# Kernel tuning notes

Hardware: AMD Instinct MI355X
Metric: run time of the kernel (lower is better)

The kernel has to match this reference:

```python
import jax, jax.numpy as jnp
import numpy as np

MAX_PEAKS = 8192        # static bound for data-dependent nonzero
HEATMAP_ALPHA = 0.9998  # alphas[0]
LOGITS_ALPHA = 0.3      # alphas[2]
WIN = 32                # window size (pad 16 on each side)
NMS_MIN2, NMS_MAX2 = 1.0, 25.0  # squared-dist band: 1 < d < 5
TOPK = (1, 1, 6, 6, 2)  # per-class selection counts from forward()
H = W = 4096


def setup_inputs() -> dict:
    key = jax.random.key(0)
    k1, k2, k3, k4, k5, k6 = jax.random.split(key, 6)
    heatmap = jax.random.uniform(k1, (H, W), dtype=jnp.float32)
    image = jax.random.normal(k2, (1, 3, H, W), dtype=jnp.float32)
    label_W = jax.random.normal(k3, (3 * WIN * WIN, 5), dtype=jnp.float32) * 0.02
    label_b = jax.random.normal(k4, (5,), dtype=jnp.float32) * 0.02
    dir_W = jax.random.normal(k5, (3 * WIN * WIN, 2), dtype=jnp.float32) * 0.02
    dir_b = jax.random.normal(k6, (2,), dtype=jnp.float32) * 0.02
    return {"heatmap": heatmap, "image": image, "label_W": label_W,
            "label_b": label_b, "dir_W": dir_W, "dir_b": dir_b}


def _clamp_alpha(x, alpha):
    x = jnp.clip(x, 0.0, 1.0)
    return jnp.where(x < alpha, 0.0, x)


def _peak_detection(hm):
    # 4-neighbor strict local maxima (same as torch shifted-slice trick)
    b = jnp.pad(hm, 1)
    c = b[1:-1, 1:-1]
    left, right = b[1:-1, 2:], b[1:-1, :-2]
    up, down = b[2:, 1:-1], b[:-2, 1:-1]
    peaks = (c > left) & (c > right) & (c > up) & (c > down)
    ys, xs = jnp.nonzero(peaks, size=MAX_PEAKS, fill_value=-1)
    valid = ys >= 0
    coords = jnp.stack([ys, xs], axis=1)  # [K,2] int, row-major like torch.nonzero
    # Original loop iterates over the ORIGINAL coords tensor (Python iterator is
    # bound before reassignment), so the suppression is order-independent:
    # drop c iff exists original peak p with 1 < dist(c,p) < 5.
    cf = coords.astype(jnp.float32)
    n2 = jnp.sum(cf * cf, axis=1)
    d2 = n2[:, None] + n2[None, :] - 2.0 * (cf @ cf.T)  # [K,K] squared dists
    reject = jnp.any((d2 > NMS_MIN2) & (d2 < NMS_MAX2) & valid[None, :], axis=1)
    return coords, valid & ~reject


def _build_windows(img, coords):
    pad = jnp.pad(img, ((0, 0), (0, 0), (16, 16), (16, 16)))
    starts = jnp.clip(coords, 0)  # padded slots (-1) read window 0; masked later
    def grab(p):
        return jax.lax.dynamic_slice(pad, (0, 0, p[0], p[1]), (1, 3, WIN, WIN))[0]
    return jax.vmap(grab)(starts)  # [K,3,32,32]


def reference(heatmap, image, label_W, label_b, dir_W, dir_b):
    hm = _clamp_alpha(heatmap, HEATMAP_ALPHA)
    coords, keep = _peak_detection(hm)
    windows = _build_windows(image, coords)            # [K,3,32,32]
    feats = windows.reshape(MAX_PEAKS, -1)             # [K,3072]
    logp = jax.nn.log_softmax(feats @ label_W + label_b, axis=-1)
    probs = jnp.exp(logp)                              # torch.exp(self.label(windows))
    scores = jnp.max(probs, axis=-1)
    labels = jnp.argmax(probs, axis=-1)
    valid = keep & (scores > LOGITS_ALPHA)
    probs_valid = probs * valid[:, None].astype(probs.dtype)  # [K,5]
    # per-class top-k (fixed k, masked with -inf instead of boolean gather)
    topk_scores, topk_idx = [], []
    for c, k in enumerate(TOPK):
        sc = jnp.where(valid & (labels == c), scores, -jnp.inf)
        v, i = jax.lax.top_k(sc, k)
        topk_scores.append(jnp.where(jnp.isfinite(v), v, 0.0))
        topk_idx.append(i)
    topk_scores = jnp.concatenate(topk_scores)          # [16]
    cue_idx = topk_idx[4]
    cue_dir = jnp.flip(feats[cue_idx] @ dir_W + dir_b, axis=0)  # [::-1] in source
    sel_peaks = coords[jnp.concatenate(topk_idx)]       # [16,2]
    return probs_valid, topk_scores, cue_dir, sel_peaks
```

## Files before the change

### kernel.cpp

```cpp
#include <hip/hip_runtime.h>
#include <math.h>
#include <stdint.h>

#define HH 4096
#define WW 4096
#define MAXP 8192
#define ALPHA_F 0.9998f
#define ROWCAP 64


__device__ __forceinline__ float clampA(float v) {
    float t = fminf(fmaxf(v, 0.f), 1.f);
    return (t < ALPHA_F) ? 0.f : t;
}

__device__ __forceinline__ unsigned long long shflx_u64(unsigned long long v, int m) {
    int lo = __shfl_xor((int)(v & 0xFFFFFFFFull), m);
    int hi = __shfl_xor((int)(v >> 32), m);
    return ((unsigned long long)(unsigned int)hi << 32) | (unsigned int)lo;
}

__global__ __launch_bounds__(256) void k_peak(const float* __restrict__ hm,
                                              unsigned short* __restrict__ xlist,
                                              int* __restrict__ rowcount) {
    int row  = blockIdx.x * 4 + (threadIdx.x >> 6);
    int lane = threadIdx.x & 63;
    const float* r = hm + (size_t)row * WW;
    const float4* r4 = (const float4*)r;
    unsigned short* xl = xlist + (size_t)row * ROWCAP;
    int cnt = 0;
    for (int ch = 0; ch < 16; ++ch) {
        int v4i = ch * 64 + lane;
        float4 v = r4[v4i];
        float c0 = clampA(v.x), c1 = clampA(v.y), c2 = clampA(v.z), c3 = clampA(v.w);
        bool any4 = (c0 > 0.f) || (c1 > 0.f) || (c2 > 0.f) || (c3 > 0.f);
        unsigned long long bb = __ballot(any4);
        if (bb == 0ull) continue;
        int pmask = 0;
        if (any4) {
            int x0 = v4i * 4;
            float lft = (x0 > 0)       ? clampA(r[x0 - 1]) : 0.f;
            float rgt = (x0 + 4 < WW)  ? clampA(r[x0 + 4]) : 0.f;
            float cc[4] = {c0, c1, c2, c3};
            float lv[4] = {lft, c0, c1, c2};
            float rv[4] = {c1, c2, c3, rgt};
            #pragma unroll
            for (int e = 0; e < 4; ++e) {
                if (cc[e] > 0.f && cc[e] > lv[e] && cc[e] > rv[e]) {
                    int x = x0 + e;
                    float up = (row > 0)      ? clampA(hm[(size_t)(row - 1) * WW + x]) : 0.f;
                    float dn = (row < HH - 1) ? clampA(hm[(size_t)(row + 1) * WW + x]) : 0.f;
                    if (cc[e] > up && cc[e] > dn) pmask |= (1 << e);
                }
            }
        }
        int pc = __popc(pmask);
        int incl = pc;
        #pragma unroll
        for (int d = 1; d < 64; d <<= 1) {
            int o = __shfl_up(incl, d);
            if (lane >= d) incl += o;
        }
        int pos = cnt + incl - pc;
        while (pmask) {
            int e = __builtin_ctz(pmask);
            if (pos < ROWCAP) xl[pos] = (unsigned short)(v4i * 4 + e);
            ++pos;
            pmask &= pmask - 1;
        }
        cnt += __shfl(incl, 63);
    }
    if (lane == 0) rowcount[row] = min(cnt, ROWCAP);
}

__global__ __launch_bounds__(1024) void k_scan(const int* __restrict__ rowcount,
                                               const unsigned short* __restrict__ xlist,
                                               int* __restrict__ Pp,
                                               int* __restrict__ cy, int* __restrict__ cx,
                                               int* __restrict__ rej) {
    __shared__ int sums[1024];
    int tid = threadIdx.x;
    int base = tid * 4;
    int a0 = rowcount[base + 0];
    int a1 = rowcount[base + 1];
    int a2 = rowcount[base + 2];
    int a3 = rowcount[base + 3];
    int s = a0 + a1 + a2 + a3;
    sums[tid] = s;
    __syncthreads();
    for (int d = 1; d < 1024; d <<= 1) {
        int v = (tid >= d) ? sums[tid - d] : 0;
        __syncthreads();
        if (tid >= d) sums[tid] += v;
        __syncthreads();
    }
    int excl = sums[tid] - s;
    int total = sums[1023];
    int P = min(total, MAXP);
    int cnts[4] = {a0, a1, a2, a3};
    int pos = excl;
    #pragma unroll
    for (int r = 0; r < 4; ++r) {
        int row = base + r;
        const unsigned short* xl = xlist + (size_t)row * ROWCAP;
        for (int t = 0; t < cnts[r]; ++t) {
            if (pos < MAXP) { cy[pos] = row; cx[pos] = (int)xl[t]; }
            ++pos;
        }
    }
    for (int i = P + tid; i < MAXP; i += 1024) { cy[i] = -1; cx[i] = -1; }
    for (int i = tid; i < MAXP; i += 1024) rej[i] = 0;
    if (tid == 0) *Pp = P;
}

__global__ __launch_bounds__(256) void k_nms(const int* __restrict__ cy,
                                             const int* __restrict__ cx,
                                             const int* __restrict__ Pp,
                                             int* __restrict__ rej) {
    int P = *Pp;
    if ((int)(blockIdx.x * 256) >= P) return;
    int jlo = blockIdx.y * 512;
    if (jlo >= P) return;
    int jhi = min(jlo + 512, P);
    __shared__ int   sy[256], sx[256];
    __shared__ float sn2[256];
    int tid = threadIdx.x;
    int i = blockIdx.x * 256 + tid;
    int yi = cy[i], xi = cx[i];
    float n2i = (float)(yi * yi + xi * xi);
    bool reject = false;
    for (int t0 = jlo; t0 < jhi; t0 += 256) {
        int lim = min(256, jhi - t0);
        if (tid < lim) {
            int yj0 = cy[t0 + tid], xj0 = cx[t0 + tid];
            sy[tid] = yj0; sx[tid] = xj0;
            sn2[tid] = (float)(yj0 * yj0 + xj0 * xj0);
        }
        __syncthreads();
        for (int u = 0; u < lim; ++u) {
            int yj = sy[u], xj = sx[u];
            float dot = (float)(yi * yj + xi * xj);
            float d2 = (n2i + sn2[u]) - 2.0f * dot;
            reject = reject || ((d2 > 1.0f) && (d2 < 25.0f));
        }
        __syncthreads();
    }
    if (reject && i < P) atomicOr(&rej[i], 1);
}

__global__ __launch_bounds__(256) void k_logits(const float* __restrict__ img,
                                                const float* __restrict__ lW,
                                                const float* __restrict__ lb,
                                                const int* __restrict__ cy,
                                                const int* __restrict__ cx,
                                                const int* __restrict__ rej,
                                                const int* __restrict__ Pp,
                                                float* __restrict__ outP,
                                                float* __restrict__ score,
                                                int* __restrict__ label,
                                                int* __restrict__ validf) {
    int tid = threadIdx.x;
    int i0 = blockIdx.x * 8;
    int P = *Pp;
    bool kp[8];
    int ys[8], xs[8];
    bool anyk = false;
    #pragma unroll
    for (int p = 0; p < 8; ++p) {
        int i = i0 + p;
        kp[p] = (i < P) && (rej[i] == 0);
        anyk |= kp[p];
        ys[p] = cy[i]; xs[p] = cx[i];
    }
    if (tid < 8) {
        int i = i0 + tid;
        bool k2 = (i < P) && (rej[i] == 0);
        if (!k2) {
            #pragma unroll
            for (int o = 0; o < 5; ++o) outP[(size_t)i * 5 + o] = 0.f;
            score[i] = 0.f; label[i] = -1; validf[i] = 0;
        }
    }
    if (!anyk) return;

    float acc[8][5];
    #pragma unroll
    for (int p = 0; p < 8; ++p)
        #pragma unroll
        for (int o = 0; o < 5; ++o) acc[p][o] = 0.f;

    for (int m = 0; m < 12; ++m) {
        int k  = tid + m * 256;
        int c  = k >> 10;
        int r  = (k >> 5) & 31;
        int wx = k & 31;
        const float* wr = lW + (size_t)k * 5;
        float w0 = wr[0], w1 = wr[1], w2 = wr[2], w3 = wr[3], w4 = wr[4];
        #pragma unroll
        for (int p = 0; p < 8; ++p) {
            if (!kp[p]) continue;
            int iy = ys[p] - 16 + r, ix = xs[p] - 16 + wx;
            float f = 0.f;
            if ((unsigned)iy < 4096u && (unsigned)ix < 4096u)
                f = img[(size_t)c * 16777216u + (size_t)iy * 4096u + (unsigned)ix];
            acc[p][0] += f * w0;
            acc[p][1] += f * w1;
            acc[p][2] += f * w2;
            acc[p][3] += f * w3;
            acc[p][4] += f * w4;
        }
    }
    __shared__ float wsum[4][8][5];
    int wid = tid >> 6, lane = tid & 63;
    #pragma unroll
    for (int p = 0; p < 8; ++p) {
        #pragma unroll
        for (int off = 32; off > 0; off >>= 1) {
            #pragma unroll
            for (int o = 0; o < 5; ++o) acc[p][o] += __shfl_xor(acc[p][o], off);
        }
        if (lane == 0) {
            #pragma unroll
            for (int o = 0; o < 5; ++o) wsum[wid][p][o] = acc[p][o];
        }
    }
    __syncthreads();
    if (tid < 8) {
        int i = i0 + tid;
        bool k2 = (i < P) && (rej[i] == 0);
        if (k2) {
            float z[5], sh[5], pr[5];
            #pragma unroll
            for (int o = 0; o < 5; ++o)
                z[o] = wsum[0][tid][o] + wsum[1][tid][o] + wsum[2][tid][o] + wsum[3][tid][o] + lb[o];
            float mx = z[0];
            #pragma unroll
            for (int o = 1; o < 5; ++o) mx = fmaxf(mx, z[o]);
            float s = 0.f;
            #pragma unroll
            for (int o = 0; o < 5; ++o) { sh[o] = z[o] - mx; s += expf(sh[o]); }
            float ls = logf(s);
            float best = -1.f; int bi = 0;
            #pragma unroll
            for (int o = 0; o < 5; ++o) {
                pr[o] = expf(sh[o] - ls);
                if (pr[o] > best) { best = pr[o]; bi = o; }
            }
            int v = (best > 0.3f) ? 1 : 0;
            #pragma unroll
            for (int o = 0; o < 5; ++o) outP[(size_t)i * 5 + o] = v ? pr[o] : 0.f;
            score[i] = best; label[i] = bi; validf[i] = v;
        }
    }
}

__global__ __launch_bounds__(256) void k_topk(const float* __restrict__ score,
                                              const int* __restrict__ label,
                                              const int* __restrict__ validf,
                                              const int* __restrict__ cy,
                                              const int* __restrict__ cx,
                                              const float* __restrict__ img,
                                              const float* __restrict__ dW,
                                              const float* __restrict__ db,
                                              float* __restrict__ out) {
    int tid = threadIdx.x;
    int wid = tid >> 6, lane = tid & 63;
    unsigned int sv[32];
    int labv[32];
    #pragma unroll
    for (int m = 0; m < 32; ++m) {
        int i = m * 256 + tid;
        float s = score[i];
        sv[m]   = validf[i] ? __float_as_uint(s) : 0u;
        labv[m] = label[i];
    }
    __shared__ unsigned long long wbest[4];
    const int KS[5] = {1, 1, 6, 6, 2};
    int outPos = 0;
    int cue0 = 0, cue1 = 0;
    for (int c = 0; c < 5; ++c) {
        unsigned long long prevKey = ~0ull;
        for (int t = 0; t < KS[c]; ++t) {
            unsigned long long best = 0;
            #pragma unroll
            for (int m = 0; m < 32; ++m) {
                int i = m * 256 + tid;
                unsigned int hi = (labv[m] == c) ? sv[m] : 0u;
                unsigned long long key =
                    ((unsigned long long)hi << 32) | (0xFFFFFFFFu - (unsigned int)i);
                if (key >= prevKey) key = 0;
                if (key > best) best = key;
            }
            #pragma unroll
            for (int off = 32; off > 0; off >>= 1) {
                unsigned long long o = shflx_u64(best, off);
                if (o > best) best = o;
            }
            if (lane == 0) wbest[wid] = best;
            __syncthreads();
            best = wbest[0];
            if (wbest[1] > best) best = wbest[1];
            if (wbest[2] > best) best = wbest[2];
            if (wbest[3] > best) best = wbest[3];
            __syncthreads();
            prevKey = best;
            int win = (int)(0xFFFFFFFFu - (unsigned int)(best & 0xFFFFFFFFull));
            if (c == 4) { if (t == 0) cue0 = win; else cue1 = win; }
            if (tid == 0) {
                unsigned int hi = (unsigned int)(best >> 32);
                out[40960 + outPos] = hi ? __uint_as_float(hi) : 0.f;
                out[40980 + outPos * 2 + 0] = (float)cy[win];
                out[40980 + outPos * 2 + 1] = (float)cx[win];
            }
            ++outPos;
        }
    }
    int cueIdx[2] = {cue0, cue1};
    #pragma unroll
    for (int s = 0; s < 2; ++s) {
        int i = (s == 0) ? cueIdx[0] : cueIdx[1];
        int y = max(cy[i], 0), x = max(cx[i], 0);
        float a0 = 0.f, a1 = 0.f;
        for (int m = 0; m < 12; ++m) {
            int k  = tid + m * 256;
            int c  = k >> 10;
            int r  = (k >> 5) & 31;
            int wx = k & 31;
            int iy = y - 16 + r, ix = x - 16 + wx;
            float f = 0.f;
            if ((unsigned)iy < 4096u && (unsigned)ix < 4096u)
                f = img[(size_t)c * 16777216u + (size_t)iy * 4096u + (unsigned)ix];
            a0 += f * dW[(size_t)k * 2 + 0];
            a1 += f * dW[(size_t)k * 2 + 1];
        }
        #pragma unroll
        for (int off = 32; off > 0; off >>= 1) {
            a0 += __shfl_xor(a0, off);
            a1 += __shfl_xor(a1, off);
        }
        __shared__ float wa[4][2];
        if (lane == 0) { wa[wid][0] = a0; wa[wid][1] = a1; }
        __syncthreads();
        if (tid == 0) {
            float s0 = wa[0][0] + wa[1][0] + wa[2][0] + wa[3][0] + db[0];
            float s1 = wa[0][1] + wa[1][1] + wa[2][1] + wa[3][1] + db[1];
            out[40976 + (1 - s) * 2 + 0] = s0;
            out[40976 + (1 - s) * 2 + 1] = s1;
        }
        __syncthreads();
    }
}

extern "C" void kernel_launch(void* const* d_in, const int* in_sizes, int n_in,
                              void* d_out, int out_size, void* d_ws, size_t ws_size,
                              hipStream_t stream) {
    const float* hm  = (const float*)d_in[0];
    const float* img = (const float*)d_in[1];
    const float* lW  = (const float*)d_in[2];
    const float* lb  = (const float*)d_in[3];
    const float* dW  = (const float*)d_in[4];
    const float* db  = (const float*)d_in[5];
    float* out = (float*)d_out;

    uint8_t* w = (uint8_t*)d_ws;
    unsigned short* xlist = (unsigned short*)(w + 0);
    int*   rowcount = (int*)  (w + 524288);
    int*   cy       = (int*)  (w + 540672);
    int*   cx       = (int*)  (w + 573440);
    int*   rej      = (int*)  (w + 606208);
    float* score    = (float*)(w + 638976);
    int*   label    = (int*)  (w + 671744);
    int*   validf   = (int*)  (w + 704512);
    int*   Pp       = (int*)  (w + 737280);

    hipLaunchKernelGGL(k_peak,   dim3(1024),   dim3(256),  0, stream, hm, xlist, rowcount);
    hipLaunchKernelGGL(k_scan,   dim3(1),      dim3(1024), 0, stream, rowcount, xlist, Pp, cy, cx, rej);
    hipLaunchKernelGGL(k_nms,    dim3(32, 16), dim3(256),  0, stream, cy, cx, Pp, rej);
    hipLaunchKernelGGL(k_logits, dim3(1024),   dim3(256),  0, stream, img, lW, lb, cy, cx, rej, Pp,
                       out, score, label, validf);
    hipLaunchKernelGGL(k_topk,   dim3(1),      dim3(256),  0, stream, score, label, validf, cy, cx,
                       img, dW, db, out);
}
```

Before: 433.8 us.

## Fuse NMS into logits kernel and split per-class top-k across waves

Measured after the change: 485.2 us. +11.8%, slower.

```diff
diff --git a/kernel.cpp b/kernel.cpp
--- a/kernel.cpp
+++ b/kernel.cpp
@@ -76,8 +76,7 @@
 __global__ __launch_bounds__(1024) void k_scan(const int* __restrict__ rowcount,
                                                const unsigned short* __restrict__ xlist,
                                                int* __restrict__ Pp,
-                                               int* __restrict__ cy, int* __restrict__ cx,
-                                               int* __restrict__ rej) {
+                                               int* __restrict__ cy, int* __restrict__ cx) {
     __shared__ int sums[1024];
     int tid = threadIdx.x;
     int base = tid * 4;
@@ -109,43 +108,7 @@
         }
     }
     for (int i = P + tid; i < MAXP; i += 1024) { cy[i] = -1; cx[i] = -1; }
-    for (int i = tid; i < MAXP; i += 1024) rej[i] = 0;
     if (tid == 0) *Pp = P;
-}
-
-__global__ __launch_bounds__(256) void k_nms(const int* __restrict__ cy,
-                                             const int* __restrict__ cx,
-                                             const int* __restrict__ Pp,
-                                             int* __restrict__ rej) {
-    int P = *Pp;
-    if ((int)(blockIdx.x * 256) >= P) return;
-    int jlo = blockIdx.y * 512;
-    if (jlo >= P) return;
-    int jhi = min(jlo + 512, P);
-    __shared__ int   sy[256], sx[256];
-    __shared__ float sn2[256];
-    int tid = threadIdx.x;
-    int i = blockIdx.x * 256 + tid;
-    int yi = cy[i], xi = cx[i];
-    float n2i = (float)(yi * yi + xi * xi);
-    bool reject = false;
-    for (int t0 = jlo; t0 < jhi; t0 += 256) {
-        int lim = min(256, jhi - t0);
-        if (tid < lim) {
-            int yj0 = cy[t0 + tid], xj0 = cx[t0 + tid];
-            sy[tid] = yj0; sx[tid] = xj0;
-            sn2[tid] = (float)(yj0 * yj0 + xj0 * xj0);
-        }
-        __syncthreads();
-        for (int u = 0; u < lim; ++u) {
-            int yj = sy[u], xj = sx[u];
-            float dot = (float)(yi * yj + xi * xj);
-            float d2 = (n2i + sn2[u]) - 2.0f * dot;
-            reject = reject || ((d2 > 1.0f) && (d2 < 25.0f));
-        }
-        __syncthreads();
-    }
-    if (reject && i < P) atomicOr(&rej[i], 1);
 }
 
 __global__ __launch_bounds__(256) void k_logits(const float* __restrict__ img,
@@ -153,32 +116,70 @@
                                                 const float* __restrict__ lb,
                                                 const int* __restrict__ cy,
                                                 const int* __restrict__ cx,
-                                                const int* __restrict__ rej,
                                                 const int* __restrict__ Pp,
                                                 float* __restrict__ outP,
-                                                float* __restrict__ score,
-                                                int* __restrict__ label,
-                                                int* __restrict__ validf) {
+                                                unsigned int* __restrict__ clskeys) {
     int tid = threadIdx.x;
     int i0 = blockIdx.x * 8;
     int P = *Pp;
-    bool kp[8];
+
+    if (i0 >= P) {
+        if (tid < 8) {
+            int i = i0 + tid;
+            #pragma unroll
+            for (int o = 0; o < 5; ++o) outP[(size_t)i * 5 + o] = 0.f;
+            #pragma unroll
+            for (int o = 0; o < 5; ++o) clskeys[o * MAXP + i] = 0u;
+        }
+        return;
+    }
+
+    bool inP[8];
     int ys[8], xs[8];
-    bool anyk = false;
     #pragma unroll
     for (int p = 0; p < 8; ++p) {
         int i = i0 + p;
-        kp[p] = (i < P) && (rej[i] == 0);
+        inP[p] = (i < P);
+        ys[p] = cy[i]; xs[p] = cx[i];
+    }
+
+    __shared__ int rejMaskS;
+    if (tid == 0) rejMaskS = 0;
+    __syncthreads();
+    float n2i[8];
+    #pragma unroll
+    for (int p = 0; p < 8; ++p)
+        n2i[p] = (float)(ys[p] * ys[p] + xs[p] * xs[p]);
+    int rbits = 0;
+    for (int j = tid; j < P; j += 256) {
+        int yj = cy[j], xj = cx[j];
+        float n2j = (float)(yj * yj + xj * xj);
+        #pragma unroll
+        for (int p = 0; p < 8; ++p) {
+            float dot = (float)(ys[p] * yj + xs[p] * xj);
+            float d2 = (n2i[p] + n2j) - 2.0f * dot;
+            if ((d2 > 1.0f) && (d2 < 25.0f)) rbits |= (1 << p);
+        }
+    }
+    if (rbits) atomicOr(&rejMaskS, rbits);
+    __syncthreads();
+    int rejMask = rejMaskS;
+
+    bool kp[8];
+    bool anyk = false;
+    #pragma unroll
+    for (int p = 0; p < 8; ++p) {
+        kp[p] = inP[p] && !((rejMask >> p) & 1);
         anyk |= kp[p];
-        ys[p] = cy[i]; xs[p] = cx[i];
     }
     if (tid < 8) {
         int i = i0 + tid;
-        bool k2 = (i < P) && (rej[i] == 0);
+        bool k2 = (i < P) && !((rejMask >> tid) & 1);
         if (!k2) {
             #pragma unroll
             for (int o = 0; o < 5; ++o) outP[(size_t)i * 5 + o] = 0.f;
-            score[i] = 0.f; label[i] = -1; validf[i] = 0;
+            #pragma unroll
+            for (int o = 0; o < 5; ++o) clskeys[o * MAXP + i] = 0u;
         }
     }
     if (!anyk) return;
@@ -227,7 +228,7 @@
     __syncthreads();
     if (tid < 8) {
         int i = i0 + tid;
-        bool k2 = (i < P) && (rej[i] == 0);
+        bool k2 = (i < P) && !((rejMask >> tid) & 1);
         if (k2) {
             float z[5], sh[5], pr[5];
             #pragma unroll
@@ -249,14 +250,15 @@
             int v = (best > 0.3f) ? 1 : 0;
             #pragma unroll
             for (int o = 0; o < 5; ++o) outP[(size_t)i * 5 + o] = v ? pr[o] : 0.f;
-            score[i] = best; label[i] = bi; validf[i] = v;
-        }
-    }
-}
-
-__global__ __launch_bounds__(256) void k_topk(const float* __restrict__ score,
-                                              const int* __restrict__ label,
-                                              const int* __restrict__ validf,
+            unsigned int sb = __float_as_uint(best);
+            #pragma unroll
+            for (int o = 0; o < 5; ++o)
+                clskeys[o * MAXP + i] = (v && bi == o) ? sb : 0u;
+        }
+    }
+}
+
+__global__ __launch_bounds__(256) void k_topk(const unsigned int* __restrict__ clskeys,
                                               const int* __restrict__ cy,
                                               const int* __restrict__ cx,
                                               const float* __restrict__ img,
@@ -265,29 +267,20 @@
                                               float* __restrict__ out) {
     int tid = threadIdx.x;
     int wid = tid >> 6, lane = tid & 63;
-    unsigned int sv[32];
-    int labv[32];
-    #pragma unroll
-    for (int m = 0; m < 32; ++m) {
-        int i = m * 256 + tid;
-        float s = score[i];
-        sv[m]   = validf[i] ? __float_as_uint(s) : 0u;
-        labv[m] = label[i];
-    }
-    __shared__ unsigned long long wbest[4];
-    const int KS[5] = {1, 1, 6, 6, 2};
-    int outPos = 0;
-    int cue0 = 0, cue1 = 0;
-    for (int c = 0; c < 5; ++c) {
+    __shared__ int cueS[2];
+    const int baseOf[5] = {0, 1, 2, 8, 14};
+    for (int a = 0; a < 2; ++a) {
+        int c, kk;
+        if (a == 0) { c = wid; kk = (wid < 2) ? 1 : 6; }
+        else { if (wid != 0) break; c = 4; kk = 2; }
+        const unsigned int* hiArr = clskeys + (size_t)c * MAXP;
         unsigned long long prevKey = ~0ull;
-        for (int t = 0; t < KS[c]; ++t) {
+        int base = baseOf[c];
+        for (int t = 0; t < kk; ++t) {
             unsigned long long best = 0;
-            #pragma unroll
-            for (int m = 0; m < 32; ++m) {
-                int i = m * 256 + tid;
-                unsigned int hi = (labv[m] == c) ? sv[m] : 0u;
-                unsigned long long key =
-                    ((unsigned long long)hi << 32) | (0xFFFFFFFFu - (unsigned int)i);
+            for (int i = lane; i < MAXP; i += 64) {
+                unsigned long long key = ((unsigned long long)hiArr[i] << 32)
+                                       | (0xFFFFFFFFu - (unsigned int)i);
                 if (key >= prevKey) key = 0;
                 if (key > best) best = key;
             }
@@ -296,29 +289,22 @@
                 unsigned long long o = shflx_u64(best, off);
                 if (o > best) best = o;
             }
-            if (lane == 0) wbest[wid] = best;
-            __syncthreads();
-            best = wbest[0];
-            if (wbest[1] > best) best = wbest[1];
-            if (wbest[2] > best) best = wbest[2];
-            if (wbest[3] > best) best = wbest[3];
-            __syncthreads();
             prevKey = best;
             int win = (int)(0xFFFFFFFFu - (unsigned int)(best & 0xFFFFFFFFull));
-            if (c == 4) { if (t == 0) cue0 = win; else cue1 = win; }
-            if (tid == 0) {
+            if (lane == 0) {
                 unsigned int hi = (unsigned int)(best >> 32);
-                out[40960 + outPos] = hi ? __uint_as_float(hi) : 0.f;
-                out[40980 + outPos * 2 + 0] = (float)cy[win];
-                out[40980 + outPos * 2 + 1] = (float)cx[win];
-            }
-            ++outPos;
-        }
-    }
-    int cueIdx[2] = {cue0, cue1};
+                int pos = base + t;
+                out[40960 + pos] = hi ? __uint_as_float(hi) : 0.f;
+                out[40980 + pos * 2 + 0] = (float)cy[win];
+                out[40980 + pos * 2 + 1] = (float)cx[win];
+                if (c == 4) cueS[t] = win;
+            }
+        }
+    }
+    __syncthreads();
     #pragma unroll
     for (int s = 0; s < 2; ++s) {
-        int i = (s == 0) ? cueIdx[0] : cueIdx[1];
+        int i = cueS[s];
         int y = max(cy[i], 0), x = max(cx[i], 0);
         float a0 = 0.f, a1 = 0.f;
         for (int m = 0; m < 12; ++m) {
@@ -363,21 +349,17 @@
     float* out = (float*)d_out;
 
     uint8_t* w = (uint8_t*)d_ws;
-    unsigned short* xlist = (unsigned short*)(w + 0);
-    int*   rowcount = (int*)  (w + 524288);
-    int*   cy       = (int*)  (w + 540672);
-    int*   cx       = (int*)  (w + 573440);
-    int*   rej      = (int*)  (w + 606208);
-    float* score    = (float*)(w + 638976);
-    int*   label    = (int*)  (w + 671744);
-    int*   validf   = (int*)  (w + 704512);
-    int*   Pp       = (int*)  (w + 737280);
-
-    hipLaunchKernelGGL(k_peak,   dim3(1024),   dim3(256),  0, stream, hm, xlist, rowcount);
-    hipLaunchKernelGGL(k_scan,   dim3(1),      dim3(1024), 0, stream, rowcount, xlist, Pp, cy, cx, rej);
-    hipLaunchKernelGGL(k_nms,    dim3(32, 16), dim3(256),  0, stream, cy, cx, Pp, rej);
-    hipLaunchKernelGGL(k_logits, dim3(1024),   dim3(256),  0, stream, img, lW, lb, cy, cx, rej, Pp,
-                       out, score, label, validf);
-    hipLaunchKernelGGL(k_topk,   dim3(1),      dim3(256),  0, stream, score, label, validf, cy, cx,
+    unsigned short* xlist  = (unsigned short*)(w + 0);
+    int*          rowcount = (int*)          (w + 524288);
+    int*          cy       = (int*)          (w + 540672);
+    int*          cx       = (int*)          (w + 573440);
+    unsigned int* clskeys  = (unsigned int*) (w + 606208);
+    int*          Pp       = (int*)          (w + 770048);
+
+    hipLaunchKernelGGL(k_peak,   dim3(1024), dim3(256),  0, stream, hm, xlist, rowcount);
+    hipLaunchKernelGGL(k_scan,   dim3(1),    dim3(1024), 0, stream, rowcount, xlist, Pp, cy, cx);
+    hipLaunchKernelGGL(k_logits, dim3(1024), dim3(256),  0, stream, img, lW, lb, cy, cx, Pp,
+                       out, clskeys);
+    hipLaunchKernelGGL(k_topk,   dim3(1),    dim3(256),  0, stream, clskeys, cy, cx,
                        img, dW, db, out);
 }
```
